# Optimization experiments

Measured on AMD Instinct MI355X. Metric: run time of the kernel, lower is better.

Reference implementation:

```python
import jax, jax.numpy as jnp
import numpy as np
from jax import lax

N_DIRS = 5
B = 8192


def setup_inputs() -> dict:
    key = jax.random.key(0)
    ks = jax.random.split(key, 7)
    return {
        "x_restored": jax.random.normal(ks[0], (B, 3, 20, 20), dtype=jnp.float32),
        "x_distorted": jax.random.normal(ks[1], (B, 5), dtype=jnp.float32),
        "w1": jax.random.normal(ks[2], (128, 5), dtype=jnp.float32) * 0.05,
        "w2": jax.random.normal(ks[3], (1200, 128), dtype=jnp.float32) * 0.05,
        "b2": jax.random.normal(ks[4], (1200,), dtype=jnp.float32) * 0.05,
        "conv_w": jax.random.normal(ks[5], (15, 6, 3, 3), dtype=jnp.float32) * 0.05,
        "conv_b": jax.random.normal(ks[6], (15,), dtype=jnp.float32) * 0.05,
    }


def gram_schmidt(x):
    # x: (B, n_dirs, d). Sequential projection-subtract chain; the projection
    # basis vectors are detached (stop_gradient) and normalized, matching torch.
    n = x.shape[1]
    outs = []
    proj = []
    for i in range(n):  # tiny fixed loop over n_dirs=5
        w = x[:, i, :]
        for wh in proj:
            w = w - wh * jnp.sum(w * wh, axis=-1, keepdims=True)
        wd = lax.stop_gradient(w)
        wh = wd / jnp.linalg.norm(wd, axis=-1, keepdims=True)
        outs.append(w)
        proj.append(wh)
    return jnp.stack(outs, axis=1)


def reference(x_restored, x_distorted, w1, w2, b2, conv_w, conv_b):
    # init_proj MLP: Linear(5,128,bias=False) -> ReLU -> Linear(128,1200)
    h = jax.nn.relu(x_distorted[:, :5] @ w1.T)           # (B,128)
    xd = (h @ w2.T + b2).reshape(x_restored.shape)        # (B,3,20,20)
    x = jnp.concatenate([xd, x_restored], axis=1)         # (B,6,20,20)
    # wrapped net: Conv2d(6 -> n_dirs*3, k=3, pad=1)
    w = lax.conv_general_dilated(
        x, conv_w, window_strides=(1, 1), padding="SAME",
        dimension_numbers=("NCHW", "OIHW", "NCHW"))
    w = w + conv_b[None, :, None, None]                   # (B,15,20,20)
    b = x_restored.shape[0]
    w = w.reshape(b, N_DIRS, 3, 20, 20)
    w_flat = w.reshape(b, N_DIRS, -1)                     # (B,5,1200)
    w_orth = gram_schmidt(w_flat)
    return w_orth.reshape(b, N_DIRS, 3, 20, 20)
```

## Files before the change

### kernel.cpp

```cpp
#include <hip/hip_runtime.h>


#define NB 8192

typedef __attribute__((ext_vector_type(8))) short short8;
typedef __attribute__((ext_vector_type(4))) float floatx4;
typedef unsigned short u16;

__device__ inline u16 f2bf(float f) {
    unsigned int u = __float_as_uint(f);
    unsigned int r = (u + 0x7FFFu + ((u >> 16) & 1u)) >> 16;
    return (u16)r;
}
__device__ inline float bf2f(u16 u) {
    return __uint_as_float(((unsigned int)u) << 16);
}

__global__ __launch_bounds__(256) void mlp1_kernel(const float* __restrict__ xdist,
                                                   const float* __restrict__ w1,
                                                   u16* __restrict__ hb) {
    int gid = blockIdx.x * 256 + threadIdx.x;
    int b = gid >> 7, j = gid & 127;
    const float* xr = xdist + b * 5;
    const float* wr = w1 + j * 5;
    float s = xr[0] * wr[0];
    s = fmaf(xr[1], wr[1], s);
    s = fmaf(xr[2], wr[2], s);
    s = fmaf(xr[3], wr[3], s);
    s = fmaf(xr[4], wr[4], s);
    hb[gid] = f2bf(fmaxf(s, 0.0f));
}

__global__ __launch_bounds__(256) void castw2_kernel(const float* __restrict__ w2,
                                                     u16* __restrict__ w2b) {
    int i = blockIdx.x * 256 + threadIdx.x;
    w2b[i] = f2bf(w2[i]);
}

__global__ __launch_bounds__(256) void mlp2_mfma(const u16* __restrict__ hb,
                                                 const u16* __restrict__ w2b,
                                                 const float* __restrict__ b2,
                                                 u16* __restrict__ xdb) {
    const int tid = threadIdx.x;
    const int lane = tid & 63, wv = tid >> 6;
    const int tile = blockIdx.x * 4 + wv;
    const int mt = tile / 25, nt = tile - mt * 25;
    const int rsel = lane & 15, kg = lane >> 4;

    short8 a[4][4], bfr[3][4];
    #pragma unroll
    for (int mi = 0; mi < 4; ++mi) {
        const u16* ap = hb + (size_t)(mt * 64 + mi * 16 + rsel) * 128 + kg * 8;
        #pragma unroll
        for (int ks = 0; ks < 4; ++ks) a[mi][ks] = *(const short8*)(ap + ks * 32);
    }
    #pragma unroll
    for (int ni = 0; ni < 3; ++ni) {
        const u16* bp = w2b + (size_t)(nt * 48 + ni * 16 + rsel) * 128 + kg * 8;
        #pragma unroll
        for (int ks = 0; ks < 4; ++ks) bfr[ni][ks] = *(const short8*)(bp + ks * 32);
    }
    floatx4 acc[4][3];
    #pragma unroll
    for (int mi = 0; mi < 4; ++mi)
        #pragma unroll
        for (int ni = 0; ni < 3; ++ni)
            acc[mi][ni] = (floatx4){0.f, 0.f, 0.f, 0.f};

    #pragma unroll
    for (int ks = 0; ks < 4; ++ks)
        #pragma unroll
        for (int mi = 0; mi < 4; ++mi)
            #pragma unroll
            for (int ni = 0; ni < 3; ++ni)
                acc[mi][ni] = __builtin_amdgcn_mfma_f32_16x16x32_bf16(
                    a[mi][ks], bfr[ni][ks], acc[mi][ni], 0, 0, 0);

    #pragma unroll
    for (int ni = 0; ni < 3; ++ni) {
        float bias = b2[nt * 48 + ni * 16 + rsel];
        #pragma unroll
        for (int mi = 0; mi < 4; ++mi) {
            #pragma unroll
            for (int r = 0; r < 4; ++r) {
                int m = mt * 64 + mi * 16 + kg * 4 + r;
                xdb[(size_t)m * 1200 + nt * 48 + ni * 16 + rsel] = f2bf(acc[mi][ni][r] + bias);
            }
        }
    }
}

#define XS2 23
#define XPL 506
#define WLS 424

__global__ __launch_bounds__(256) void conv_gs_kernel(const u16* __restrict__ xdb,
                                                      const float* __restrict__ xres,
                                                      const float* __restrict__ cw,
                                                      const float* __restrict__ cb,
                                                      float* __restrict__ out) {
    const int b = blockIdx.x;
    const int tid = threadIdx.x;
    const int lane = tid & 63, wv = tid >> 6;
    const int rsel = lane & 15, kg = lane >> 4;
    __shared__ __align__(16) u16 xpad[3040];
    __shared__ __align__(16) u16 wl16[16 * WLS];
    __shared__ float Gsh[16 * 17];
    __shared__ float Ash[12];

    short8 bf0, bf1;
    #pragma unroll
    for (int j = 0; j < 8; ++j) {
        int k0 = kg * 8 + j;
        int k1 = 32 + kg * 8 + j;
        float v0 = (rsel < 15 && k0 < 54) ? cw[rsel * 54 + k0] : 0.f;
        float v1 = (rsel < 15 && k1 < 54) ? cw[rsel * 54 + k1] : 0.f;
        bf0[j] = (short)f2bf(v0);
        bf1[j] = (short)f2bf(v1);
    }
    const float bias = cb[rsel < 15 ? rsel : 14];
    int offA[16];
    #pragma unroll
    for (int q = 0; q < 16; ++q) {
        int k = (q >> 3) * 32 + kg * 8 + (q & 7);
        int ci = k / 9, tap = k - ci * 9, dy = tap / 3, dx = tap - dy * 3;
        offA[q] = (k < 54) ? (ci * XPL + dy * XS2 + dx) : 0;
    }

    unsigned int* xz = (unsigned int*)xpad;
    #pragma unroll
    for (int i2 = 0; i2 < 6; ++i2) {
        int i = tid + i2 * 256;
        if (i < 1520) xz[i] = 0u;
    }
    if (tid < 180) {
        int row = tid / 12, d = tid % 12;
        ((unsigned int*)wl16)[row * 212 + 200 + d] = 0u;
    }
    __syncthreads();

    const u16* s0 = xdb + (size_t)b * 1200;
    const float* s1 = xres + (size_t)b * 1200;
    #pragma unroll
    for (int i2 = 0; i2 < 5; ++i2) {
        int i = tid + i2 * 256;
        if (i < 1200) {
            int c = i / 400, p = i - c * 400, y = p / 20, x = p - y * 20;
            xpad[c * XPL + (y + 1) * XS2 + (x + 1)] = s0[i];
        }
    }
    #pragma unroll
    for (int i2 = 0; i2 < 5; ++i2) {
        int i = tid + i2 * 256;
        if (i < 1200) {
            int c = i / 400 + 3, p = i % 400, y = p / 20, x = p - (p / 20) * 20;
            xpad[c * XPL + (y + 1) * XS2 + (x + 1)] = f2bf(s1[i]);
        }
    }
    __syncthreads();

    for (int t = wv; t < 25; t += 4) {
        const int px = t * 16 + rsel;
        const int y = px / 20;
        const int pb = y * XS2 + (px - y * 20);
        short8 a0, a1;
        #pragma unroll
        for (int j = 0; j < 8; ++j) a0[j] = (short)xpad[pb + offA[j]];
        #pragma unroll
        for (int j = 0; j < 8; ++j) a1[j] = (short)xpad[pb + offA[8 + j]];
        floatx4 acc = (floatx4){bias, bias, bias, bias};
        acc = __builtin_amdgcn_mfma_f32_16x16x32_bf16(a0, bf0, acc, 0, 0, 0);
        acc = __builtin_amdgcn_mfma_f32_16x16x32_bf16(a1, bf1, acc, 0, 0, 0);
        if (rsel < 15) {
            unsigned int lo, hi;
            asm volatile("v_cvt_pk_bf16_f32 %0, %1, %2" : "=v"(lo) : "v"(acc[0]), "v"(acc[1]));
            asm volatile("v_cvt_pk_bf16_f32 %0, %1, %2" : "=v"(hi) : "v"(acc[2]), "v"(acc[3]));
            *(uint2*)(wl16 + rsel * WLS + t * 16 + kg * 4) = make_uint2(lo, hi);
        }
    }
    __syncthreads();

    if (wv == 0) {
        floatx4 gacc = (floatx4){0.f, 0.f, 0.f, 0.f};
        #pragma unroll
        for (int s = 0; s < 13; ++s) {
            short8 f = *(const short8*)(wl16 + rsel * WLS + s * 32 + kg * 8);
            gacc = __builtin_amdgcn_mfma_f32_16x16x32_bf16(f, f, gacc, 0, 0, 0);
        }
        #pragma unroll
        for (int r = 0; r < 4; ++r)
            Gsh[(kg * 4 + r) * 17 + rsel] = gacc[r];

        float Gd[5][5];
        #pragma unroll
        for (int d = 0; d < 5; ++d)
            #pragma unroll
            for (int e = 0; e < 5; ++e)
                Gd[d][e] = Gsh[(3 * d) * 17 + 3 * e] +
                           Gsh[(3 * d + 1) * 17 + 3 * e + 1] +
                           Gsh[(3 * d + 2) * 17 + 3 * e + 2];

        float A[5][5];
        #pragma unroll
        for (int i = 0; i < 5; ++i)
            #pragma unroll
            for (int j = 0; j < 5; ++j) A[i][j] = (i == j) ? 1.f : 0.f;
        #pragma unroll
        for (int j = 0; j < 4; ++j) {
            float v[5];
            #pragma unroll
            for (int rr = 0; rr < 5; ++rr) {
                float s0a = 0.f;
                #pragma unroll
                for (int k = 0; k < 5; ++k)
                    if (k <= j) s0a = fmaf(A[j][k], Gd[k][rr], s0a);
                v[rr] = s0a;
            }
            float dj = 0.f;
            #pragma unroll
            for (int k = 0; k < 5; ++k)
                if (k <= j) dj = fmaf(A[j][k], v[k], dj);
            float rd = 1.0f / dj;
            #pragma unroll
            for (int i = j + 1; i < 5; ++i) {
                float cij = 0.f;
                #pragma unroll
                for (int k = 0; k < 5; ++k)
                    if (k <= i) cij = fmaf(A[i][k], v[k], cij);
                cij *= rd;
                #pragma unroll
                for (int k = 0; k < 5; ++k)
                    if (k <= j) A[i][k] = fmaf(-cij, A[j][k], A[i][k]);
            }
        }
        if (tid == 0) {
            Ash[0] = A[1][0];
            Ash[1] = A[2][0]; Ash[2] = A[2][1];
            Ash[3] = A[3][0]; Ash[4] = A[3][1]; Ash[5] = A[3][2];
            Ash[6] = A[4][0]; Ash[7] = A[4][1]; Ash[8] = A[4][2]; Ash[9] = A[4][3];
        }
    }
    __syncthreads();

    if (tid < 200) {
        float a10[10];
        #pragma unroll
        for (int q = 0; q < 10; ++q) a10[q] = Ash[q];
        float* ob = out + (size_t)b * 6000;
        #pragma unroll
        for (int pp = 0; pp < 2; ++pp) {
            const int pos = tid + pp * 200;
            #pragma unroll
            for (int cc = 0; cc < 3; ++cc) {
                float w0 = bf2f(wl16[(0 + cc) * WLS + pos]);
                float w1 = bf2f(wl16[(3 + cc) * WLS + pos]);
                float w2v = bf2f(wl16[(6 + cc) * WLS + pos]);
                float w3 = bf2f(wl16[(9 + cc) * WLS + pos]);
                float w4 = bf2f(wl16[(12 + cc) * WLS + pos]);
                float u4 = fmaf(a10[9], w3, fmaf(a10[8], w2v, fmaf(a10[7], w1, fmaf(a10[6], w0, w4))));
                float u3 = fmaf(a10[5], w2v, fmaf(a10[4], w1, fmaf(a10[3], w0, w3)));
                float u2 = fmaf(a10[2], w1, fmaf(a10[1], w0, w2v));
                float u1 = fmaf(a10[0], w0, w1);
                ob[(0 + cc) * 400 + pos] = w0;
                ob[(3 + cc) * 400 + pos] = u1;
                ob[(6 + cc) * 400 + pos] = u2;
                ob[(9 + cc) * 400 + pos] = u3;
                ob[(12 + cc) * 400 + pos] = u4;
            }
        }
    }
}

extern "C" void kernel_launch(void* const* d_in, const int* in_sizes, int n_in,
                              void* d_out, int out_size, void* d_ws, size_t ws_size,
                              hipStream_t stream) {
    const float* x_restored  = (const float*)d_in[0];
    const float* x_distorted = (const float*)d_in[1];
    const float* w1          = (const float*)d_in[2];
    const float* w2          = (const float*)d_in[3];
    const float* b2          = (const float*)d_in[4];
    const float* conv_w      = (const float*)d_in[5];
    const float* conv_b      = (const float*)d_in[6];
    float* out = (float*)d_out;

    u16* xdb = (u16*)d_ws;
    u16* hb  = xdb + (size_t)NB * 1200;
    u16* w2b = hb + (size_t)NB * 128;

    mlp1_kernel<<<(NB * 128) / 256, 256, 0, stream>>>(x_distorted, w1, hb);
    castw2_kernel<<<(1200 * 128) / 256, 256, 0, stream>>>(w2, w2b);
    mlp2_mfma<<<(128 * 25) / 4, 256, 0, stream>>>(hb, w2b, b2, xdb);
    conv_gs_kernel<<<NB, 256, 0, stream>>>(xdb, x_restored, conv_w, conv_b, out);
}
```

Measured before the change: 107.8 us.

## Pad conv tile for dword loads, compute Gram per wave, drop block syncs

```diff
diff --git a/kernel.cpp b/kernel.cpp
--- a/kernel.cpp
+++ b/kernel.cpp
@@ -90,8 +90,9 @@
     }
 }
 
-#define XS2 23
-#define XPL 506
+#define XS2 24
+#define XPL 528
+#define XPLD 264
 #define WLS 424
 
 __global__ __launch_bounds__(256) void conv_gs_kernel(const u16* __restrict__ xdb,
@@ -103,10 +104,8 @@
     const int tid = threadIdx.x;
     const int lane = tid & 63, wv = tid >> 6;
     const int rsel = lane & 15, kg = lane >> 4;
-    __shared__ __align__(16) u16 xpad[3040];
+    __shared__ __align__(16) u16 xpad[6 * XPL];
     __shared__ __align__(16) u16 wl16[16 * WLS];
-    __shared__ float Gsh[16 * 17];
-    __shared__ float Ash[12];
 
     short8 bf0, bf1;
     #pragma unroll
@@ -129,32 +128,47 @@
 
     unsigned int* xz = (unsigned int*)xpad;
     #pragma unroll
-    for (int i2 = 0; i2 < 6; ++i2) {
+    for (int i2 = 0; i2 < 2; ++i2) {
         int i = tid + i2 * 256;
-        if (i < 1520) xz[i] = 0u;
+        if (i < 264) {
+            int pl = i / 44, d = i - pl * 44;
+            int dw;
+            if (d < 12) dw = d;
+            else if (d < 24) dw = 252 + (d - 12);
+            else dw = (d - 23) * 12 + 11;
+            xz[pl * XPLD + dw] = 0u;
+        }
+    }
+    if (tid < 120) {
+        int pl = tid / 20, r = tid % 20 + 1;
+        xpad[pl * XPL + r * 24 + 1] = 0;
     }
     if (tid < 180) {
         int row = tid / 12, d = tid % 12;
         ((unsigned int*)wl16)[row * 212 + 200 + d] = 0u;
     }
-    __syncthreads();
-
-    const u16* s0 = xdb + (size_t)b * 1200;
-    const float* s1 = xres + (size_t)b * 1200;
-    #pragma unroll
-    for (int i2 = 0; i2 < 5; ++i2) {
+
+    const unsigned int* s0d = (const unsigned int*)(xdb + (size_t)b * 1200);
+    const float2* s1d = (const float2*)(xres + (size_t)b * 1200);
+    #pragma unroll
+    for (int i2 = 0; i2 < 3; ++i2) {
         int i = tid + i2 * 256;
-        if (i < 1200) {
-            int c = i / 400, p = i - c * 400, y = p / 20, x = p - y * 20;
-            xpad[c * XPL + (y + 1) * XS2 + (x + 1)] = s0[i];
-        }
-    }
-    #pragma unroll
-    for (int i2 = 0; i2 < 5; ++i2) {
+        if (i < 600) {
+            int c = i / 200, rem = i - c * 200;
+            int p = rem * 2, y = p / 20, x = p - (p / 20) * 20;
+            xz[c * XPLD + (y + 1) * 12 + (x + 2) / 2] = s0d[i];
+        }
+    }
+    #pragma unroll
+    for (int i2 = 0; i2 < 3; ++i2) {
         int i = tid + i2 * 256;
-        if (i < 1200) {
-            int c = i / 400 + 3, p = i % 400, y = p / 20, x = p - (p / 20) * 20;
-            xpad[c * XPL + (y + 1) * XS2 + (x + 1)] = f2bf(s1[i]);
+        if (i < 600) {
+            int c = i / 200, rem = i - c * 200;
+            int p = rem * 2, y = p / 20, x = p - (p / 20) * 20;
+            float2 v = s1d[i];
+            unsigned int pk;
+            asm volatile("v_cvt_pk_bf16_f32 %0, %1, %2" : "=v"(pk) : "v"(v.x), "v"(v.y));
+            xz[(3 + c) * XPLD + (y + 1) * 12 + (x + 2) / 2] = pk;
         }
     }
     __syncthreads();
@@ -162,7 +176,7 @@
     for (int t = wv; t < 25; t += 4) {
         const int px = t * 16 + rsel;
         const int y = px / 20;
-        const int pb = y * XS2 + (px - y * 20);
+        const int pb = y * XS2 + (px - y * 20) + 1;
         short8 a0, a1;
         #pragma unroll
         for (int j = 0; j < 8; ++j) a0[j] = (short)xpad[pb + offA[j]];
@@ -180,7 +194,8 @@
     }
     __syncthreads();
 
-    if (wv == 0) {
+    float* Gw = ((float*)xpad) + wv * 272;
+    {
         floatx4 gacc = (floatx4){0.f, 0.f, 0.f, 0.f};
         #pragma unroll
         for (int s = 0; s < 13; ++s) {
@@ -189,67 +204,61 @@
         }
         #pragma unroll
         for (int r = 0; r < 4; ++r)
-            Gsh[(kg * 4 + r) * 17 + rsel] = gacc[r];
-
-        float Gd[5][5];
-        #pragma unroll
-        for (int d = 0; d < 5; ++d)
-            #pragma unroll
-            for (int e = 0; e < 5; ++e)
-                Gd[d][e] = Gsh[(3 * d) * 17 + 3 * e] +
-                           Gsh[(3 * d + 1) * 17 + 3 * e + 1] +
-                           Gsh[(3 * d + 2) * 17 + 3 * e + 2];
-
-        float A[5][5];
-        #pragma unroll
-        for (int i = 0; i < 5; ++i)
-            #pragma unroll
-            for (int j = 0; j < 5; ++j) A[i][j] = (i == j) ? 1.f : 0.f;
-        #pragma unroll
-        for (int j = 0; j < 4; ++j) {
-            float v[5];
-            #pragma unroll
-            for (int rr = 0; rr < 5; ++rr) {
-                float s0a = 0.f;
-                #pragma unroll
-                for (int k = 0; k < 5; ++k)
-                    if (k <= j) s0a = fmaf(A[j][k], Gd[k][rr], s0a);
-                v[rr] = s0a;
-            }
-            float dj = 0.f;
+            Gw[(kg * 4 + r) * 17 + rsel] = gacc[r];
+    }
+    float Gd[5][5];
+    #pragma unroll
+    for (int d = 0; d < 5; ++d)
+        #pragma unroll
+        for (int e = 0; e < 5; ++e)
+            Gd[d][e] = Gw[(3 * d) * 17 + 3 * e] +
+                       Gw[(3 * d + 1) * 17 + 3 * e + 1] +
+                       Gw[(3 * d + 2) * 17 + 3 * e + 2];
+
+    float A[5][5];
+    #pragma unroll
+    for (int i = 0; i < 5; ++i)
+        #pragma unroll
+        for (int j = 0; j < 5; ++j) A[i][j] = (i == j) ? 1.f : 0.f;
+    #pragma unroll
+    for (int j = 0; j < 4; ++j) {
+        float v[5];
+        #pragma unroll
+        for (int rr = 0; rr < 5; ++rr) {
+            float s0a = 0.f;
             #pragma unroll
             for (int k = 0; k < 5; ++k)
-                if (k <= j) dj = fmaf(A[j][k], v[k], dj);
-            float rd = 1.0f / dj;
-            #pragma unroll
-            for (int i = j + 1; i < 5; ++i) {
-                float cij = 0.f;
-                #pragma unroll
-                for (int k = 0; k < 5; ++k)
-                    if (k <= i) cij = fmaf(A[i][k], v[k], cij);
-                cij *= rd;
-                #pragma unroll
-                for (int k = 0; k < 5; ++k)
-                    if (k <= j) A[i][k] = fmaf(-cij, A[j][k], A[i][k]);
-            }
-        }
-        if (tid == 0) {
-            Ash[0] = A[1][0];
-            Ash[1] = A[2][0]; Ash[2] = A[2][1];
-            Ash[3] = A[3][0]; Ash[4] = A[3][1]; Ash[5] = A[3][2];
-            Ash[6] = A[4][0]; Ash[7] = A[4][1]; Ash[8] = A[4][2]; Ash[9] = A[4][3];
-        }
-    }
-    __syncthreads();
-
-    if (tid < 200) {
-        float a10[10];
-        #pragma unroll
-        for (int q = 0; q < 10; ++q) a10[q] = Ash[q];
-        float* ob = out + (size_t)b * 6000;
-        #pragma unroll
-        for (int pp = 0; pp < 2; ++pp) {
-            const int pos = tid + pp * 200;
+                if (k <= j) s0a = fmaf(A[j][k], Gd[k][rr], s0a);
+            v[rr] = s0a;
+        }
+        float dj = 0.f;
+        #pragma unroll
+        for (int k = 0; k < 5; ++k)
+            if (k <= j) dj = fmaf(A[j][k], v[k], dj);
+        float rd = 1.0f / dj;
+        #pragma unroll
+        for (int i = j + 1; i < 5; ++i) {
+            float cij = 0.f;
+            #pragma unroll
+            for (int k = 0; k < 5; ++k)
+                if (k <= i) cij = fmaf(A[i][k], v[k], cij);
+            cij *= rd;
+            #pragma unroll
+            for (int k = 0; k < 5; ++k)
+                if (k <= j) A[i][k] = fmaf(-cij, A[j][k], A[i][k]);
+        }
+    }
+    float a10[10];
+    a10[0] = A[1][0];
+    a10[1] = A[2][0]; a10[2] = A[2][1];
+    a10[3] = A[3][0]; a10[4] = A[3][1]; a10[5] = A[3][2];
+    a10[6] = A[4][0]; a10[7] = A[4][1]; a10[8] = A[4][2]; a10[9] = A[4][3];
+
+    float* ob = out + (size_t)b * 6000;
+    #pragma unroll
+    for (int pp = 0; pp < 2; ++pp) {
+        if (pp == 0 || tid < 144) {
+            const int pos = tid + pp * 256;
             #pragma unroll
             for (int cc = 0; cc < 3; ++cc) {
                 float w0 = bf2f(wl16[(0 + cc) * WLS + pos]);
```

Result: faster. 92.15 us (-14.5%).
